# Kernel tuning notes

Measured on AMD Instinct MI355X. Metric: run time of the kernel, lower is better.

Reference implementation:

```python
import jax, jax.numpy as jnp
import numpy as np

N, E, IN, H, C = 50000, 1600000, 256, 256, 2


def _lin(k, o, i):
    return (jax.random.normal(k, (o, i), jnp.float32) / np.sqrt(i)).astype(jnp.float32)


def setup_inputs() -> dict:
    key = jax.random.key(0)
    ks = jax.random.split(key, 16)
    x = jax.random.normal(ks[0], (N, IN), jnp.float32)
    edge_index = jax.random.randint(ks[1], (2, E), 0, N, dtype=jnp.int32)
    return dict(
        x=x, edge_index=edge_index,
        W1=_lin(ks[2], H, IN), b1=0.01 * jax.random.normal(ks[10], (H,), jnp.float32),
        W2=_lin(ks[3], H, H), b2=0.01 * jax.random.normal(ks[11], (H,), jnp.float32),
        W3=_lin(ks[4], H, H), b3=0.01 * jax.random.normal(ks[12], (H,), jnp.float32),
        W4=_lin(ks[5], C, H), b4=0.01 * jax.random.normal(ks[13], (C,), jnp.float32),
        T10=_lin(ks[6], H, H), T11=_lin(ks[7], H, H), cb1=0.01 * jax.random.normal(ks[14], (H,), jnp.float32),
        T20=_lin(ks[8], H, H), T21=_lin(ks[9], H, H), cb2=0.01 * jax.random.normal(ks[15], (H,), jnp.float32),
    )


def _cheb_norm(edge_index, n):
    # PyG ChebConv, normalization='sym', lambda_max=2.0:
    # L_hat = 2/lambda_max * (I - D^-1/2 A D^-1/2) - I = -D^-1/2 A D^-1/2
    # (the +I and -I self-loop terms cancel), so only off-diagonal norm remains.
    row, col = edge_index[0], edge_index[1]
    deg = jax.ops.segment_sum(jnp.ones((edge_index.shape[1],), jnp.float32), row, num_segments=n)
    dis = jnp.where(deg > 0, jax.lax.rsqrt(jnp.where(deg > 0, deg, 1.0)), 0.0)
    return -dis[row] * dis[col]  # [E]


def _cheb_conv(x, edge_index, norm, W0, W1, b, n):
    # K=2: out = Tx_0 @ W0^T + Tx_1 @ W1^T + b, Tx_0 = x, Tx_1 = L_hat x
    src, dst = edge_index[0], edge_index[1]  # message: x_j from src, aggregate at dst
    tx1 = jax.ops.segment_sum(norm[:, None] * x[src], dst, num_segments=n)
    return x @ W0.T + tx1 @ W1.T + b


def reference(x, edge_index, W1, b1, W2, b2, W3, b3, W4, b4, T10, T11, cb1, T20, T21, cb2):
    n = x.shape[0]
    norm = _cheb_norm(edge_index, n)
    h = jax.nn.relu(x @ W1.T + b1)
    h = jax.nn.relu(h @ W2.T + b2)
    h = _cheb_conv(h, edge_index, norm, T10, T11, cb1, n)
    h = _cheb_conv(h, edge_index, norm, T20, T21, cb2, n)
    h = jax.nn.relu(h @ W3.T + b3)
    return h @ W4.T + b4
```

## Files before the change

### kernel.cpp

```cpp
#include <hip/hip_runtime.h>

#define HDIM 256
#define NHB 256
#define NBINB 50048
#define NBINW (NBINB/4)

typedef __attribute__((ext_vector_type(8))) short short8v;
typedef __attribute__((ext_vector_type(4))) short short4v;
typedef __attribute__((ext_vector_type(4))) float floatx4;

static __device__ __forceinline__ unsigned short f2bf(float f) {
    union { float f; unsigned u; } c; c.f = f;
    unsigned u = c.u;
    unsigned r = u + 0x7FFFu + ((u >> 16) & 1u);
    return (unsigned short)(r >> 16);
}
static __device__ __forceinline__ float bf2f(unsigned short h) {
    union { unsigned u; float f; } c; c.u = ((unsigned)h) << 16;
    return c.f;
}


__global__ __launch_bounds__(512) void hist_k(const int* __restrict__ src, const int* __restrict__ dst,
                                              unsigned int* __restrict__ degS, unsigned int* __restrict__ cntS,
                                              int nE) {
    __shared__ unsigned int h8[NBINW];
    const int tid = threadIdx.x;
    const int isDst = blockIdx.x >= NHB;
    const int bb = isDst ? blockIdx.x - NHB : blockIdx.x;
    const int* __restrict__ arr = isDst ? dst : src;
    unsigned int* __restrict__ outS = isDst ? cntS : degS;

    for (int i = tid; i < NBINW; i += 512) h8[i] = 0u;
    __syncthreads();
    const int chunk = (nE + NHB - 1) / NHB;
    const int e0 = bb * chunk;
    const int e1 = min(e0 + chunk, nE);
    for (int e = e0 + tid; e < e1; e += 512) {
        int n = arr[e];
        atomicAdd(&h8[n >> 2], 1u << ((n & 3) << 3));
    }
    __syncthreads();
    unsigned int* __restrict__ row = outS + (size_t)bb * NBINW;
    for (int i = tid; i < NBINW; i += 512) row[i] = h8[i];
}


__global__ __launch_bounds__(256) void reduce_k(const unsigned char* __restrict__ degS,
                                                unsigned char* __restrict__ cntS,
                                                float* __restrict__ dis, int* __restrict__ cnt, int nN) {
    int n = blockIdx.x * 256 + threadIdx.x;
    if (n >= nN) return;
    int d = 0;
    #pragma unroll 8
    for (int b = 0; b < NHB; ++b) d += degS[(size_t)b * NBINB + n];
    dis[n] = (d > 0) ? (1.0f / sqrtf((float)d)) : 0.0f;
    unsigned run = 0;
    #pragma unroll 4
    for (int b = 0; b < NHB; ++b) {
        size_t o = (size_t)b * NBINB + n;
        unsigned t = cntS[o];
        cntS[o] = (unsigned char)run;
        run += t;
    }
    cnt[n] = (int)run;
}


__global__ __launch_bounds__(256) void scan1_k(const int* __restrict__ cnt, int* __restrict__ tmp,
                                               int* __restrict__ bsums, int nN) {
    __shared__ int s[256];
    int t = threadIdx.x;
    int i = blockIdx.x * 256 + t;
    int v = (i < nN) ? cnt[i] : 0;
    s[t] = v; __syncthreads();
    #pragma unroll
    for (int off = 1; off < 256; off <<= 1) {
        int x = (t >= off) ? s[t - off] : 0;
        __syncthreads();
        s[t] += x;
        __syncthreads();
    }
    if (i < nN) tmp[i] = s[t];
    if (t == 255) bsums[blockIdx.x] = s[255];
}

__global__ __launch_bounds__(256) void scan2_k(int* __restrict__ bsums, int nb) {
    __shared__ int s[256];
    int t = threadIdx.x;
    int v = (t < nb) ? bsums[t] : 0;
    s[t] = v; __syncthreads();
    #pragma unroll
    for (int off = 1; off < 256; off <<= 1) {
        int x = (t >= off) ? s[t - off] : 0;
        __syncthreads();
        s[t] += x;
        __syncthreads();
    }
    if (t < nb) bsums[t] = s[t] - v;
}

__global__ __launch_bounds__(256) void scan3_k(const int* __restrict__ cnt, const int* __restrict__ tmp,
                                               const int* __restrict__ bsums, int* __restrict__ offs,
                                               int nN, int nE) {
    int i = blockIdx.x * 256 + threadIdx.x;
    if (i < nN) offs[i] = tmp[i] - cnt[i] + bsums[blockIdx.x];
    if (i == nN - 1) offs[nN] = nE;
}


__global__ __launch_bounds__(512) void fill_k(const int* __restrict__ src, const int* __restrict__ dst,
                                              const float* __restrict__ dis, const int* __restrict__ offs,
                                              const unsigned int* __restrict__ cntS,
                                              int2* __restrict__ csr, int nE) {
    __shared__ unsigned int cur8[NBINW];
    const int tid = threadIdx.x;
    const int bb = blockIdx.x;
    const unsigned int* __restrict__ baseRow = cntS + (size_t)bb * NBINW;
    for (int i = tid; i < NBINW; i += 512) cur8[i] = baseRow[i];
    __syncthreads();
    const int chunk = (nE + NHB - 1) / NHB;
    const int e0 = bb * chunk;
    const int e1 = min(e0 + chunk, nE);
    for (int e = e0 + tid; e < e1; e += 512) {
        int s = src[e], d = dst[e];
        unsigned sh = (unsigned)(d & 3) << 3;
        unsigned old = atomicAdd(&cur8[d >> 2], 1u << sh);
        unsigned c = (old >> sh) & 0xFFu;
        int p = offs[d] + (int)c;
        float w = -dis[s] * dis[d];
        csr[p] = make_int2(s, __float_as_int(w));
    }
}


struct WPtrs { const float* w[7]; };
__global__ __launch_bounds__(256) void wsplit_all_k(WPtrs ws, unsigned short* __restrict__ base) {
    int wi = blockIdx.x >> 6;
    int idx = (blockIdx.x & 63) * 256 + threadIdx.x;
    const float* w = ws.w[wi];
    unsigned short* hi = base + (size_t)wi * 131072;
    unsigned short* lo = hi + 65536;
    float4 v = ((const float4*)w)[idx];
    float f[4] = {v.x, v.y, v.z, v.w};
    short4v hv, lv;
    #pragma unroll
    for (int e = 0; e < 4; ++e) {
        unsigned short h = f2bf(f[e]);
        float rem = f[e] - bf2f(h);
        hv[e] = (short)h;
        lv[e] = (short)f2bf(rem);
    }
    *(short4v*)(hi + idx * 4) = hv;
    *(short4v*)(lo + idx * 4) = lv;
}


#define LDP 40

__global__ __launch_bounds__(512, 4) void mfma_gemm_k(
    const float* __restrict__ AF,
    const unsigned short* __restrict__ Ah0, const unsigned short* __restrict__ Al0,
    const unsigned short* __restrict__ Wh0, const unsigned short* __restrict__ Wl0,
    const unsigned short* __restrict__ Ah1, const unsigned short* __restrict__ Al1,
    const unsigned short* __restrict__ Wh1, const unsigned short* __restrict__ Wl1,
    const float* __restrict__ bias,
    float* __restrict__ outF, unsigned short* __restrict__ outHi, unsigned short* __restrict__ outLo,
    int nRows, int relu, int dual)
{
    __shared__ short Ahs[128 * LDP];
    __shared__ short Als[128 * LDP];
    __shared__ short Bhs[256 * LDP];
    __shared__ short Bls[256 * LDP];

    const int tid  = threadIdx.x;
    const int lane = tid & 63;
    const int wv   = tid >> 6;
    const int wm   = wv >> 2, wn = wv & 3;
    const int lrow = lane & 15, kg = lane >> 4;
    const int row0 = blockIdx.x * 128;

    const int sr = tid >> 2, sc = tid & 3;
    int agr = row0 + sr; if (agr >= nRows) agr = nRows - 1;

    floatx4 acc[4][4];
    #pragma unroll
    for (int i = 0; i < 4; ++i)
        #pragma unroll
        for (int j = 0; j < 4; ++j)
            acc[i][j] = (floatx4)0.0f;

    const int npass = dual ? 2 : 1;
    for (int pass = 0; pass < npass; ++pass) {
        const unsigned short* __restrict__ Ah = pass ? Ah1 : Ah0;
        const unsigned short* __restrict__ Al = pass ? Al1 : Al0;
        const unsigned short* __restrict__ Wh = pass ? Wh1 : Wh0;
        const unsigned short* __restrict__ Wl = pass ? Wl1 : Wl0;
        const bool f32A = (pass == 0) && (AF != nullptr);
        for (int k0 = 0; k0 < HDIM; k0 += 32) {
            __syncthreads();
            if (f32A) {
                const float* pa = AF + (size_t)agr * HDIM + k0 + sc * 8;
                float4 v0 = *(const float4*)pa;
                float4 v1 = *(const float4*)(pa + 4);
                float f[8] = {v0.x, v0.y, v0.z, v0.w, v1.x, v1.y, v1.z, v1.w};
                short8v hv, lv;
                #pragma unroll
                for (int e = 0; e < 8; ++e) {
                    unsigned short h = f2bf(f[e]);
                    float rem = f[e] - bf2f(h);
                    hv[e] = (short)h;
                    lv[e] = (short)f2bf(rem);
                }
                *(short8v*)(Ahs + sr * LDP + sc * 8) = hv;
                *(short8v*)(Als + sr * LDP + sc * 8) = lv;
            } else {
                size_t ga = (size_t)agr * HDIM + k0 + sc * 8;
                *(short8v*)(Ahs + sr * LDP + sc * 8) = *(const short8v*)(Ah + ga);
                *(short8v*)(Als + sr * LDP + sc * 8) = *(const short8v*)(Al + ga);
            }
            #pragma unroll
            for (int q = 0; q < 2; ++q) {
                int idx = tid + q * 512;
                int br = idx >> 2, bc = idx & 3;
                size_t gb = (size_t)br * HDIM + k0 + bc * 8;
                *(short8v*)(Bhs + br * LDP + bc * 8) = *(const short8v*)(Wh + gb);
                *(short8v*)(Bls + br * LDP + bc * 8) = *(const short8v*)(Wl + gb);
            }
            __syncthreads();

            short8v ahf[4], alf[4];
            #pragma unroll
            for (int fm = 0; fm < 4; ++fm) {
                int ra = (wm * 64 + fm * 16 + lrow) * LDP + kg * 8;
                ahf[fm] = *(const short8v*)(Ahs + ra);
                alf[fm] = *(const short8v*)(Als + ra);
            }
            #pragma unroll
            for (int fn = 0; fn < 4; ++fn) {
                int rb = (wn * 64 + fn * 16 + lrow) * LDP + kg * 8;
                short8v bh = *(const short8v*)(Bhs + rb);
                short8v bl = *(const short8v*)(Bls + rb);
                #pragma unroll
                for (int fm = 0; fm < 4; ++fm) {
                    acc[fm][fn] = __builtin_amdgcn_mfma_f32_16x16x32_bf16(ahf[fm], bh, acc[fm][fn], 0, 0, 0);
                    acc[fm][fn] = __builtin_amdgcn_mfma_f32_16x16x32_bf16(ahf[fm], bl, acc[fm][fn], 0, 0, 0);
                    acc[fm][fn] = __builtin_amdgcn_mfma_f32_16x16x32_bf16(alf[fm], bh, acc[fm][fn], 0, 0, 0);
                }
            }
        }
    }

    #pragma unroll
    for (int fn = 0; fn < 4; ++fn) {
        int col = wn * 64 + fn * 16 + lrow;
        float bv = bias[col];
        #pragma unroll
        for (int fm = 0; fm < 4; ++fm) {
            #pragma unroll
            for (int r = 0; r < 4; ++r) {
                int grow = row0 + wm * 64 + fm * 16 + kg * 4 + r;
                if (grow < nRows) {
                    float v = acc[fm][fn][r] + bv;
                    if (relu) v = fmaxf(v, 0.0f);
                    size_t o = (size_t)grow * HDIM + col;
                    if (outF) outF[o] = v;
                    if (outHi) {
                        unsigned short h = f2bf(v);
                        outHi[o] = h;
                        outLo[o] = f2bf(v - bf2f(h));
                    }
                }
            }
        }
    }
}


__global__ __launch_bounds__(256) void aggregate_k(
    const unsigned short* __restrict__ hb, const int2* __restrict__ csr,
    const int* __restrict__ offs,
    unsigned short* __restrict__ outHi, unsigned short* __restrict__ outLo)
{
    const int n = blockIdx.x;
    const int t = threadIdx.x;
    const int start = offs[n], end = offs[n + 1];
    float acc = 0.0f;
    int e = start;
    for (; e + 8 <= end; e += 8) {
        int2 ee[8];
        #pragma unroll
        for (int q = 0; q < 8; ++q) ee[q] = csr[e + q];
        unsigned short hv[8];
        #pragma unroll
        for (int q = 0; q < 8; ++q) hv[q] = hb[(size_t)ee[q].x * HDIM + t];
        #pragma unroll
        for (int q = 0; q < 8; ++q) acc = fmaf(__int_as_float(ee[q].y), bf2f(hv[q]), acc);
    }
    for (; e < end; ++e) {
        int2 ee = csr[e];
        acc = fmaf(__int_as_float(ee.y), bf2f(hb[(size_t)ee.x * HDIM + t]), acc);
    }
    size_t o = (size_t)n * HDIM + t;
    unsigned short h = f2bf(acc);
    outHi[o] = h;
    outLo[o] = f2bf(acc - bf2f(h));
}


__global__ __launch_bounds__(256) void final_k(const float* __restrict__ h, const float* __restrict__ W4,
                                               const float* __restrict__ b4, float* __restrict__ out, int nN) {
    int gid = blockIdx.x * 256 + threadIdx.x;
    int wid = gid >> 6;
    int lane = threadIdx.x & 63;
    if (wid >= nN) return;
    float4 v  = *(const float4*)(h + (size_t)wid * HDIM + lane * 4);
    float4 w0 = *(const float4*)(W4 + lane * 4);
    float4 w1 = *(const float4*)(W4 + HDIM + lane * 4);
    float d0 = v.x * w0.x + v.y * w0.y + v.z * w0.z + v.w * w0.w;
    float d1 = v.x * w1.x + v.y * w1.y + v.z * w1.z + v.w * w1.w;
    #pragma unroll
    for (int off = 32; off > 0; off >>= 1) {
        d0 += __shfl_down(d0, off, 64);
        d1 += __shfl_down(d1, off, 64);
    }
    if (lane == 0) {
        out[(size_t)wid * 2 + 0] = d0 + b4[0];
        out[(size_t)wid * 2 + 1] = d1 + b4[1];
    }
}


extern "C" void kernel_launch(void* const* d_in, const int* in_sizes, int n_in,
                              void* d_out, int out_size, void* d_ws, size_t ws_size,
                              hipStream_t stream) {
    const float* x   = (const float*)d_in[0];
    const int*   ei  = (const int*)d_in[1];
    const float* W1  = (const float*)d_in[2];
    const float* b1  = (const float*)d_in[3];
    const float* W2  = (const float*)d_in[4];
    const float* b2  = (const float*)d_in[5];
    const float* W3  = (const float*)d_in[6];
    const float* b3  = (const float*)d_in[7];
    const float* W4  = (const float*)d_in[8];
    const float* b4  = (const float*)d_in[9];
    const float* T10 = (const float*)d_in[10];
    const float* T11 = (const float*)d_in[11];
    const float* cb1 = (const float*)d_in[12];
    const float* T20 = (const float*)d_in[13];
    const float* T21 = (const float*)d_in[14];
    const float* cb2 = (const float*)d_in[15];

    const int nN = in_sizes[0] / HDIM;
    const int nE = in_sizes[1] / 2;
    const int* src = ei;
    const int* dst = ei + nE;

    char* p = (char*)d_ws;
    auto alloc = [&](size_t bytes) { void* r = (void*)p; p += (bytes + 255) & ~(size_t)255; return r; };
    float* dis     = (float*)alloc((size_t)nN * 4);
    int*   cnt     = (int*)alloc((size_t)nN * 4);
    int*   tmp     = (int*)alloc((size_t)nN * 4);
    int*   bsums   = (int*)alloc(1024 * 4);
    int*   offs    = (int*)alloc((size_t)(nN + 1) * 4);
    int2*  csr     = (int2*)alloc((size_t)nE * 8);
    unsigned int* degS = (unsigned int*)alloc((size_t)NHB * NBINB);
    unsigned int* cntS = (unsigned int*)alloc((size_t)NHB * NBINB);
    const size_t NH = (size_t)nN * HDIM;
    unsigned short* Xh  = (unsigned short*)alloc(NH * 4);  unsigned short* Xl  = Xh + NH;
    unsigned short* Ahp = (unsigned short*)alloc(NH * 4);  unsigned short* Alp = Ahp + NH;
    unsigned short* Bhp = (unsigned short*)alloc(NH * 4);  unsigned short* Blp = Bhp + NH;
    unsigned short* Dhp = (unsigned short*)alloc(NH * 4);  unsigned short* Dlp = Dhp + NH;
    unsigned short* wsp = (unsigned short*)alloc((size_t)7 * 131072 * 2);
    float* bufF = (float*)Xh;

    float* out = (float*)d_out;
    const int nbN = (nN + 255) / 256;

    hist_k<<<2 * NHB, 512, 0, stream>>>(src, dst, degS, cntS, nE);
    reduce_k<<<nbN, 256, 0, stream>>>((const unsigned char*)degS, (unsigned char*)cntS, dis, cnt, nN);
    scan1_k<<<nbN, 256, 0, stream>>>(cnt, tmp, bsums, nN);
    scan2_k<<<1, 256, 0, stream>>>(bsums, nbN);
    scan3_k<<<nbN, 256, 0, stream>>>(cnt, tmp, bsums, offs, nN, nE);
    fill_k<<<NHB, 512, 0, stream>>>(src, dst, dis, offs, cntS, csr, nE);

    WPtrs wp; wp.w[0]=W1; wp.w[1]=W2; wp.w[2]=T10; wp.w[3]=T11; wp.w[4]=T20; wp.w[5]=T21; wp.w[6]=W3;
    wsplit_all_k<<<7 * 64, 256, 0, stream>>>(wp, wsp);
    unsigned short* wh[7]; unsigned short* wl[7];
    for (int i = 0; i < 7; ++i) { wh[i] = wsp + (size_t)i * 131072; wl[i] = wh[i] + 65536; }

    const int gb = (nN + 127) / 128;

    mfma_gemm_k<<<gb, 512, 0, stream>>>(x, nullptr, nullptr, wh[0], wl[0],
                                        nullptr, nullptr, nullptr, nullptr,
                                        b1, nullptr, Ahp, Alp, nN, 1, 0);
    mfma_gemm_k<<<gb, 512, 0, stream>>>(nullptr, Ahp, Alp, wh[1], wl[1],
                                        nullptr, nullptr, nullptr, nullptr,
                                        b2, nullptr, Bhp, Blp, nN, 1, 0);

    aggregate_k<<<nN, 256, 0, stream>>>(Bhp, csr, offs, Xh, Xl);
    mfma_gemm_k<<<gb, 512, 0, stream>>>(nullptr, Bhp, Blp, wh[2], wl[2],
                                        Xh, Xl, wh[3], wl[3],
                                        cb1, nullptr, Dhp, Dlp, nN, 0, 1);

    aggregate_k<<<nN, 256, 0, stream>>>(Dhp, csr, offs, Ahp, Alp);
    mfma_gemm_k<<<gb, 512, 0, stream>>>(nullptr, Dhp, Dlp, wh[4], wl[4],
                                        Ahp, Alp, wh[5], wl[5],
                                        cb2, nullptr, Bhp, Blp, nN, 0, 1);

    mfma_gemm_k<<<gb, 512, 0, stream>>>(nullptr, Bhp, Blp, wh[6], wl[6],
                                        nullptr, nullptr, nullptr, nullptr,
                                        b3, bufF, nullptr, nullptr, nN, 1, 0);
    final_k<<<(nN + 3) / 4, 256, 0, stream>>>(bufF, W4, b4, out, nN);
}
```

Measured before the change: 653.8 us.

## Split neighbor aggregation across four wavefronts with vectorized bf16 row loads

The per-node aggregation kernel now has each of its four wavefronts handle a strided subset of the incoming edges. Each lane loads four bf16 features as one 8-byte load instead of a 2-byte load per thread. Partial sums are combined through shared memory plus a barrier before the hi/lo bf16 split is written. This aims to raise memory-level parallelism and shorten the serial per-edge loop of the gather-bound kernel, at the cost of LDS traffic, a sync, and a changed floating-point summation order.

```diff
diff --git a/kernel.cpp b/kernel.cpp
--- a/kernel.cpp
+++ b/kernel.cpp
@@ -282,29 +282,61 @@
     const int* __restrict__ offs,
     unsigned short* __restrict__ outHi, unsigned short* __restrict__ outLo)
 {
+    __shared__ float red[4][256];
     const int n = blockIdx.x;
+    const int w = threadIdx.x >> 6;
+    const int lane = threadIdx.x & 63;
+    const int start = offs[n], end = offs[n + 1];
+
+    float a0 = 0.f, a1 = 0.f, a2 = 0.f, a3 = 0.f;
+    int e = start + w;
+    for (; e + 12 < end; e += 16) {
+        int2 m0 = csr[e], m1 = csr[e + 4], m2 = csr[e + 8], m3 = csr[e + 12];
+        const uint2 g0 = *(const uint2*)(hb + (size_t)m0.x * HDIM + lane * 4);
+        const uint2 g1 = *(const uint2*)(hb + (size_t)m1.x * HDIM + lane * 4);
+        const uint2 g2 = *(const uint2*)(hb + (size_t)m2.x * HDIM + lane * 4);
+        const uint2 g3 = *(const uint2*)(hb + (size_t)m3.x * HDIM + lane * 4);
+        float w0 = __int_as_float(m0.y), w1 = __int_as_float(m1.y);
+        float w2 = __int_as_float(m2.y), w3 = __int_as_float(m3.y);
+        a0 = fmaf(w0, __uint_as_float(g0.x << 16), a0);
+        a1 = fmaf(w0, __uint_as_float(g0.x & 0xffff0000u), a1);
+        a2 = fmaf(w0, __uint_as_float(g0.y << 16), a2);
+        a3 = fmaf(w0, __uint_as_float(g0.y & 0xffff0000u), a3);
+        a0 = fmaf(w1, __uint_as_float(g1.x << 16), a0);
+        a1 = fmaf(w1, __uint_as_float(g1.x & 0xffff0000u), a1);
+        a2 = fmaf(w1, __uint_as_float(g1.y << 16), a2);
+        a3 = fmaf(w1, __uint_as_float(g1.y & 0xffff0000u), a3);
+        a0 = fmaf(w2, __uint_as_float(g2.x << 16), a0);
+        a1 = fmaf(w2, __uint_as_float(g2.x & 0xffff0000u), a1);
+        a2 = fmaf(w2, __uint_as_float(g2.y << 16), a2);
+        a3 = fmaf(w2, __uint_as_float(g2.y & 0xffff0000u), a3);
+        a0 = fmaf(w3, __uint_as_float(g3.x << 16), a0);
+        a1 = fmaf(w3, __uint_as_float(g3.x & 0xffff0000u), a1);
+        a2 = fmaf(w3, __uint_as_float(g3.y << 16), a2);
+        a3 = fmaf(w3, __uint_as_float(g3.y & 0xffff0000u), a3);
+    }
+    for (; e < end; e += 4) {
+        int2 m = csr[e];
+        const uint2 g = *(const uint2*)(hb + (size_t)m.x * HDIM + lane * 4);
+        float wt = __int_as_float(m.y);
+        a0 = fmaf(wt, __uint_as_float(g.x << 16), a0);
+        a1 = fmaf(wt, __uint_as_float(g.x & 0xffff0000u), a1);
+        a2 = fmaf(wt, __uint_as_float(g.y << 16), a2);
+        a3 = fmaf(wt, __uint_as_float(g.y & 0xffff0000u), a3);
+    }
+
+    red[w][lane * 4 + 0] = a0;
+    red[w][lane * 4 + 1] = a1;
+    red[w][lane * 4 + 2] = a2;
+    red[w][lane * 4 + 3] = a3;
+    __syncthreads();
+
     const int t = threadIdx.x;
-    const int start = offs[n], end = offs[n + 1];
-    float acc = 0.0f;
-    int e = start;
-    for (; e + 8 <= end; e += 8) {
-        int2 ee[8];
-        #pragma unroll
-        for (int q = 0; q < 8; ++q) ee[q] = csr[e + q];
-        unsigned short hv[8];
-        #pragma unroll
-        for (int q = 0; q < 8; ++q) hv[q] = hb[(size_t)ee[q].x * HDIM + t];
-        #pragma unroll
-        for (int q = 0; q < 8; ++q) acc = fmaf(__int_as_float(ee[q].y), bf2f(hv[q]), acc);
-    }
-    for (; e < end; ++e) {
-        int2 ee = csr[e];
-        acc = fmaf(__int_as_float(ee.y), bf2f(hb[(size_t)ee.x * HDIM + t]), acc);
-    }
+    float s = red[0][t] + red[1][t] + red[2][t] + red[3][t];
     size_t o = (size_t)n * HDIM + t;
-    unsigned short h = f2bf(acc);
+    unsigned short h = f2bf(s);
     outHi[o] = h;
-    outLo[o] = f2bf(acc - bf2f(h));
+    outLo[o] = f2bf(s - bf2f(h));
 }
 
 
```

New measurement: 634.4 us. 3.0% less time.

## Restructure SpMM aggregation into column-sliced wavefronts with edge-parallel lanes

Applied to the files above, without the earlier changes.

Each node's aggregation moves from one 256-thread block (one bf16 channel per thread) to one wavefront per node per 32-channel slice. Within the wave, 16 lanes each read a packed pair of bf16 channels and 4 lane groups split the edges, with a shuffle reduction at the end. The aim is wider per-lane loads, more edge-level parallelism and fewer redundant CSR reads per block, so the gather is more memory-efficient. The cost is that each neighbour row is now fetched as eight separate 64-byte pieces by different blocks, which can hurt locality, and the grid becomes larger.

```diff
diff --git a/kernel.cpp b/kernel.cpp
--- a/kernel.cpp
+++ b/kernel.cpp
@@ -280,31 +280,51 @@
 __global__ __launch_bounds__(256) void aggregate_k(
     const unsigned short* __restrict__ hb, const int2* __restrict__ csr,
     const int* __restrict__ offs,
-    unsigned short* __restrict__ outHi, unsigned short* __restrict__ outLo)
+    unsigned short* __restrict__ outHi, unsigned short* __restrict__ outLo, int nN)
 {
-    const int n = blockIdx.x;
-    const int t = threadIdx.x;
+    const int slice = blockIdx.x & 7;
+    const int grp   = blockIdx.x >> 3;
+    const int w     = threadIdx.x >> 6;
+    const int n     = grp * 4 + w;
+    if (n >= nN) return;
+    const int lane = threadIdx.x & 63;
+    const int sub  = lane >> 4;
+    const int ch2  = lane & 15;
     const int start = offs[n], end = offs[n + 1];
-    float acc = 0.0f;
-    int e = start;
-    for (; e + 8 <= end; e += 8) {
-        int2 ee[8];
-        #pragma unroll
-        for (int q = 0; q < 8; ++q) ee[q] = csr[e + q];
-        unsigned short hv[8];
-        #pragma unroll
-        for (int q = 0; q < 8; ++q) hv[q] = hb[(size_t)ee[q].x * HDIM + t];
-        #pragma unroll
-        for (int q = 0; q < 8; ++q) acc = fmaf(__int_as_float(ee[q].y), bf2f(hv[q]), acc);
-    }
-    for (; e < end; ++e) {
-        int2 ee = csr[e];
-        acc = fmaf(__int_as_float(ee.y), bf2f(hb[(size_t)ee.x * HDIM + t]), acc);
-    }
-    size_t o = (size_t)n * HDIM + t;
-    unsigned short h = f2bf(acc);
-    outHi[o] = h;
-    outLo[o] = f2bf(acc - bf2f(h));
+
+    const unsigned short* __restrict__ hbs = hb + slice * 32 + ch2 * 2;
+
+    float a0 = 0.f, a1 = 0.f;
+    int e = start + sub;
+    for (; e + 4 < end; e += 8) {
+        int2 m0 = csr[e];
+        int2 m1 = csr[e + 4];
+        unsigned g0 = *(const unsigned*)(hbs + (size_t)m0.x * HDIM);
+        unsigned g1 = *(const unsigned*)(hbs + (size_t)m1.x * HDIM);
+        float w0 = __int_as_float(m0.y), w1 = __int_as_float(m1.y);
+        a0 = fmaf(w0, __uint_as_float(g0 << 16), a0);
+        a1 = fmaf(w0, __uint_as_float(g0 & 0xffff0000u), a1);
+        a0 = fmaf(w1, __uint_as_float(g1 << 16), a0);
+        a1 = fmaf(w1, __uint_as_float(g1 & 0xffff0000u), a1);
+    }
+    if (e < end) {
+        int2 m = csr[e];
+        unsigned g = *(const unsigned*)(hbs + (size_t)m.x * HDIM);
+        float wt = __int_as_float(m.y);
+        a0 = fmaf(wt, __uint_as_float(g << 16), a0);
+        a1 = fmaf(wt, __uint_as_float(g & 0xffff0000u), a1);
+    }
+
+    a0 += __shfl_xor(a0, 16, 64);  a1 += __shfl_xor(a1, 16, 64);
+    a0 += __shfl_xor(a0, 32, 64);  a1 += __shfl_xor(a1, 32, 64);
+
+    if (sub == 0) {
+        unsigned short h0 = f2bf(a0), h1 = f2bf(a1);
+        unsigned short l0 = f2bf(a0 - bf2f(h0)), l1 = f2bf(a1 - bf2f(h1));
+        size_t o = (size_t)n * HDIM + slice * 32 + ch2 * 2;
+        *(unsigned*)(outHi + o) = (unsigned)h0 | ((unsigned)h1 << 16);
+        *(unsigned*)(outLo + o) = (unsigned)l0 | ((unsigned)l1 << 16);
+    }
 }
 
 
@@ -376,6 +396,7 @@
 
     float* out = (float*)d_out;
     const int nbN = (nN + 255) / 256;
+    const int aggGrid = ((nN + 3) / 4) * 8;
 
     hist_k<<<2 * NHB, 512, 0, stream>>>(src, dst, degS, cntS, nE);
     reduce_k<<<nbN, 256, 0, stream>>>((const unsigned char*)degS, (unsigned char*)cntS, dis, cnt, nN);
@@ -398,12 +419,12 @@
                                         nullptr, nullptr, nullptr, nullptr,
                                         b2, nullptr, Bhp, Blp, nN, 1, 0);
 
-    aggregate_k<<<nN, 256, 0, stream>>>(Bhp, csr, offs, Xh, Xl);
+    aggregate_k<<<aggGrid, 256, 0, stream>>>(Bhp, csr, offs, Xh, Xl, nN);
     mfma_gemm_k<<<gb, 512, 0, stream>>>(nullptr, Bhp, Blp, wh[2], wl[2],
                                         Xh, Xl, wh[3], wl[3],
                                         cb1, nullptr, Dhp, Dlp, nN, 0, 1);
 
-    aggregate_k<<<nN, 256, 0, stream>>>(Dhp, csr, offs, Ahp, Alp);
+    aggregate_k<<<aggGrid, 256, 0, stream>>>(Dhp, csr, offs, Ahp, Alp, nN);
     mfma_gemm_k<<<gb, 512, 0, stream>>>(nullptr, Dhp, Dlp, wh[4], wl[4],
                                         Ahp, Alp, wh[5], wl[5],
                                         cb2, nullptr, Bhp, Blp, nN, 0, 1);
```

Result: slower. 855.8 us (+30.9%).
